# Kernel tuning notes

Hardware: AMD Instinct MI355X
Metric: run time of the kernel (lower is better)

Reference implementation:

```python
import jax, jax.numpy as jnp
import numpy as np
from jax import lax

B, C, T = 8, 512, 4096
K = 3
DILATIONS = (1, 3, 5)
EPS_Q = 1e-5
EPS_SNAKE = 1e-9


def quantize_weight(w):
    # BitNet-1.58-style ternary quantization with per-tensor absmean scale,
    # applied with a straight-through estimator.
    s = jnp.mean(jnp.abs(w))
    wq = jnp.clip(jnp.round(w / (s + EPS_Q)), -1.0, 1.0) * s
    return w + lax.stop_gradient(wq - w)


def bitconv1d(x, w, b, dilation, padding):
    # x: [B, C, T], w: [Cout, Cin, K], b: [Cout]
    y = lax.conv_general_dilated(
        x, quantize_weight(w),
        window_strides=(1,),
        padding=[(padding, padding)],
        rhs_dilation=(dilation,),
        dimension_numbers=("NCH", "OIH", "NCH"),
    )
    return y + b[None, :, None]


def snake_beta(x, alpha_p, beta_p):
    # log-scale parametrization: alpha = exp(alpha_p), beta = exp(beta_p)
    a = jnp.exp(alpha_p)[None, :, None]
    b = jnp.exp(beta_p)[None, :, None]
    return x + (1.0 / (b + EPS_SNAKE)) * jnp.sin(a * x) ** 2


def setup_inputs() -> dict:
    key = jax.random.key(0)
    ks = jax.random.split(key, 7)
    return {
        "x": jax.random.normal(ks[0], (B, C, T), dtype=jnp.float32),
        "w1": jax.random.normal(ks[1], (3, C, C, K), dtype=jnp.float32) * 0.05,
        "b1": jax.random.normal(ks[2], (3, C), dtype=jnp.float32) * 0.01,
        "alpha": jax.random.normal(ks[3], (3, C), dtype=jnp.float32) * 0.1,
        "beta": jax.random.normal(ks[4], (3, C), dtype=jnp.float32) * 0.1,
        "w2": jax.random.normal(ks[5], (3, C, C, K), dtype=jnp.float32) * 0.05,
        "b2": jax.random.normal(ks[6], (3, C), dtype=jnp.float32) * 0.01,
    }


def reference(x, w1, b1, alpha, beta, w2, b2):
    for i, d in enumerate(DILATIONS):
        pad1 = d * (K - 1) // 2
        h = bitconv1d(x, w1[i], b1[i], dilation=d, padding=pad1)
        h = snake_beta(h, alpha[i], beta[i])
        h = bitconv1d(h, w2[i], b2[i], dilation=1, padding=(K - 1) // 2)
        x = x + h
    return x
```

## Files before the change

kernel.cpp:

```cpp
#include <hip/hip_runtime.h>
#include <math.h>
#include <stdint.h>


constexpr int B_ = 8, C_ = 512, T_ = 4096, K_ = 3;
constexpr int WELEM = C_ * C_ * K_;

typedef __bf16 bf16x8 __attribute__((ext_vector_type(8)));
typedef float f32x4 __attribute__((ext_vector_type(4)));
typedef unsigned short u16x8 __attribute__((ext_vector_type(8)));

constexpr size_t OFF_PART = 0;
constexpr size_t OFF_S = 4096;
constexpr size_t OFF_AE = 8192;
constexpr size_t OFF_IB = 16384;
constexpr size_t OFF_WQ1 = 32768;
constexpr size_t OFF_WQ2 = OFF_WQ1 + (size_t)3 * WELEM * 2;
constexpr size_t NBCT = (size_t)B_ * C_ * T_;
constexpr size_t OFF_PHI = OFF_WQ2 + (size_t)3 * WELEM * 2;
constexpr size_t OFF_PLO = OFF_PHI + NBCT * 2;
constexpr size_t OFF_QHI = OFF_PLO + NBCT * 2;
constexpr size_t OFF_QLO = OFF_QHI + NBCT * 2;
constexpr size_t OFF_ZERO = OFF_QLO + NBCT * 2;

__device__ inline unsigned short bf16_rne(float v) {
  unsigned int u = __builtin_bit_cast(unsigned int, v);
  unsigned int r = u + 0x7FFFu + ((u >> 16) & 1u);
  return (unsigned short)(r >> 16);
}

__global__ __launch_bounds__(256)
void absmean_partial(const float* __restrict__ w1, const float* __restrict__ w2,
                     float* __restrict__ part) {
  __shared__ float red[256];
  const int t = blockIdx.y;
  const float* src = (t < 3) ? (w1 + (size_t)t * WELEM) : (w2 + (size_t)(t - 3) * WELEM);
  const int base = blockIdx.x * (256 * 32);
  float v = 0.f;
#pragma unroll
  for (int j = 0; j < 32; ++j) v += fabsf(src[base + j * 256 + threadIdx.x]);
  red[threadIdx.x] = v;
  __syncthreads();
  for (int s = 128; s > 0; s >>= 1) {
    if (threadIdx.x < (unsigned)s) red[threadIdx.x] += red[threadIdx.x + s];
    __syncthreads();
  }
  if (threadIdx.x == 0) part[t * 96 + blockIdx.x] = red[0];
}

__global__ __launch_bounds__(128)
void absmean_final(const float* __restrict__ part, float* __restrict__ svec) {
  __shared__ float red[128];
  const int t = blockIdx.x;
  red[threadIdx.x] = (threadIdx.x < 96) ? part[t * 96 + threadIdx.x] : 0.f;
  __syncthreads();
  for (int s = 64; s > 0; s >>= 1) {
    if (threadIdx.x < (unsigned)s) red[threadIdx.x] += red[threadIdx.x + s];
    __syncthreads();
  }
  if (threadIdx.x == 0) svec[t] = red[0] / (float)WELEM;
}

__global__ __launch_bounds__(256)
void quantize_kernel(const float* __restrict__ src, unsigned short* __restrict__ dst,
                     const float* __restrict__ svec, int sbase) {
  const int idx = blockIdx.x * 256 + threadIdx.x;
  const int j = idx & 7;
  const int lane = (idx >> 3) & 63;
  const int cot = (idx >> 9) & 31;
  const int rest = idx >> 14;
  const int tap = rest % 3;
  const int rest2 = rest / 3;
  const int cc = rest2 & 15;
  const int st = rest2 >> 4;
  const int co = cot * 16 + (lane & 15);
  const int ci = cc * 32 + (lane >> 4) * 8 + j;
  const float s = svec[sbase + st];
  const float w = src[(((size_t)st * C_ + co) * C_ + ci) * K_ + tap];
  float q = rintf(w / (s + 1e-5f));
  q = fminf(1.f, fmaxf(-1.f, q));
  dst[idx] = (unsigned short)(__builtin_bit_cast(unsigned int, q) >> 16);
}

__global__ __launch_bounds__(256)
void snake_params_kernel(const float* __restrict__ al, const float* __restrict__ be,
                         float* __restrict__ ae, float* __restrict__ ib,
                         float* __restrict__ zr) {
  const int idx = blockIdx.x * 256 + threadIdx.x;
  if (idx < 3 * C_) {
    ae[idx] = expf(al[idx]);
    ib[idx] = 1.f / (expf(be[idx]) + 1e-9f);
  }
  if (idx < 1024) zr[idx] = 0.f;
}

__global__ __launch_bounds__(256)
void transpose_split(const float* __restrict__ X, unsigned short* __restrict__ Hi,
                     unsigned short* __restrict__ Lo) {
  __shared__ float tile[64][68];
  const int b = blockIdx.z;
  const int c0 = blockIdx.y * 64;
  const int t0 = blockIdx.x * 64;
  const int tid = threadIdx.x;
  {
    const int cl = tid >> 2, tg = tid & 3;
    const float* src = X + ((size_t)b * C_ + c0 + cl) * T_ + t0 + tg * 16;
    float4 v0 = *(const float4*)(src);
    float4 v1 = *(const float4*)(src + 4);
    float4 v2 = *(const float4*)(src + 8);
    float4 v3 = *(const float4*)(src + 12);
    float* d = &tile[cl][tg * 16];
    *(float4*)(d) = v0; *(float4*)(d + 4) = v1;
    *(float4*)(d + 8) = v2; *(float4*)(d + 12) = v3;
  }
  __syncthreads();
  {
    const int tl = tid >> 2, cg = tid & 3;
    u16x8 h0, h1, l0, l1;
#pragma unroll
    for (int j = 0; j < 16; ++j) {
      const float v = tile[cg * 16 + j][tl];
      const unsigned short hb = bf16_rne(v);
      const float hf = __builtin_bit_cast(float, (unsigned int)hb << 16);
      const unsigned short lb = bf16_rne(v - hf);
      if (j < 8) { h0[j] = hb; l0[j] = lb; }
      else       { h1[j - 8] = hb; l1[j - 8] = lb; }
    }
    const size_t off = ((size_t)b * T_ + t0 + tl) * C_ + c0 + cg * 16;
    *(u16x8*)(Hi + off) = h0; *(u16x8*)(Hi + off + 8) = h1;
    *(u16x8*)(Lo + off) = l0; *(u16x8*)(Lo + off + 8) = l1;
  }
}

template <int DIL, bool SNAKE, bool PLANES, bool WF32>
__global__ __launch_bounds__(256, 2)
void conv_mfma(const unsigned short* __restrict__ Xhi,
               const unsigned short* __restrict__ Xlo,
               const unsigned short* __restrict__ Wq,
               unsigned int zoff,
               const float* __restrict__ svec,
               const float* __restrict__ bias, const float* __restrict__ aexp,
               const float* __restrict__ invb,
               const float* __restrict__ res,
               float* __restrict__ Y,
               unsigned short* __restrict__ Ohi,
               unsigned short* __restrict__ Olo) {
  constexpr int TT = 256;
  constexpr int R = TT + 2 * DIL;
  constexpr int R8 = (R + 7) & ~7;
  constexpr int W8 = R8 / 8;
  constexpr int NW = (W8 + 3) / 4;
  __shared__ unsigned short Xs[2][R8 * 64];

  const int b = blockIdx.z;
  const int co0 = blockIdx.y * 128;
  const int cob = blockIdx.y * 8;
  const int t0 = blockIdx.x * TT;
  const int tid = threadIdx.x;
  const int lane = tid & 63;
  const int wv = tid >> 6;
  const int l15 = lane & 15;
  const int quad = lane >> 4;

  f32x4 acc[8][4] = {};

  const size_t xbase = (size_t)b * T_ * C_;
  const unsigned int plo_delta = (unsigned int)(NBCT * 2);
  const char* xh8 = (const char*)Xhi;

  unsigned int offs[NW];
#pragma unroll
  for (int j = 0; j < NW; ++j) {
    const int wnd = wv + j * 4;
    const int rl = wnd * 8 + (lane >> 3);
    const int cpr = (lane & 7) ^ (rl & 7);
    const int p = cpr >> 2, g = cpr & 3;
    const int t = t0 - DIL + rl;
    unsigned int o;
    if (wnd < W8 && (unsigned)t < (unsigned)T_)
      o = (p ? plo_delta : 0u) + (unsigned int)((xbase + (size_t)t * C_ + g * 8) * 2);
    else
      o = zoff + (unsigned int)(g * 16);
    offs[j] = o;
  }

  auto stage = [&](int cc, int buf) {
#pragma unroll
    for (int j = 0; j < NW; ++j) {
      const int wnd = wv + j * 4;
      if (wnd < W8) {
        const char* gp = xh8 + offs[j] + cc * 64;
        __builtin_amdgcn_global_load_lds(
            (const __attribute__((address_space(1))) unsigned int*)gp,
            (__attribute__((address_space(3))) unsigned int*)&Xs[buf][wnd * 512],
            16, 0, 0);
      }
    }
  };

  stage(0, 0);
  __syncthreads();

#pragma unroll 1
  for (int cc = 0; cc < C_ / 32; ++cc) {
    const int cur = cc & 1;

    bf16x8 a0[8];
    {
      const unsigned short* wb =
          Wq + (((size_t)cc * K_ + 0) * 32 + cob) * 512 + (size_t)lane * 8;
#pragma unroll
      for (int m = 0; m < 8; ++m)
        a0[m] = __builtin_bit_cast(bf16x8, *(const u16x8*)(wb + m * 512));
    }

    if (cc < C_ / 32 - 1) stage(cc + 1, 1 - cur);

#pragma unroll
    for (int n = 0; n < 4; ++n) {
      const int r = wv * 64 + n * 16 + l15;
      const int rw = (r & 7) * 8;
      const bf16x8 bh =
          __builtin_bit_cast(bf16x8, *(const u16x8*)&Xs[cur][r * 64 + ((quad * 8) ^ rw)]);
      const bf16x8 bl =
          __builtin_bit_cast(bf16x8, *(const u16x8*)&Xs[cur][r * 64 + ((quad * 8 + 32) ^ rw)]);
#pragma unroll
      for (int m = 0; m < 8; ++m) {
        acc[m][n] = __builtin_amdgcn_mfma_f32_16x16x32_bf16(a0[m], bh, acc[m][n], 0, 0, 0);
        acc[m][n] = __builtin_amdgcn_mfma_f32_16x16x32_bf16(a0[m], bl, acc[m][n], 0, 0, 0);
      }
    }

#pragma unroll
    for (int tap = 1; tap < K_; ++tap) {
      const unsigned short* wb =
          Wq + (((size_t)cc * K_ + tap) * 32 + cob) * 512 + (size_t)lane * 8;
      bf16x8 a[8];
#pragma unroll
      for (int m = 0; m < 8; ++m)
        a[m] = __builtin_bit_cast(bf16x8, *(const u16x8*)(wb + m * 512));
#pragma unroll
      for (int n = 0; n < 4; ++n) {
        const int r = wv * 64 + n * 16 + l15 + tap * DIL;
        const int rw = (r & 7) * 8;
        const bf16x8 bh =
            __builtin_bit_cast(bf16x8, *(const u16x8*)&Xs[cur][r * 64 + ((quad * 8) ^ rw)]);
        const bf16x8 bl =
            __builtin_bit_cast(bf16x8, *(const u16x8*)&Xs[cur][r * 64 + ((quad * 8 + 32) ^ rw)]);
#pragma unroll
        for (int m = 0; m < 8; ++m) {
          acc[m][n] = __builtin_amdgcn_mfma_f32_16x16x32_bf16(a[m], bh, acc[m][n], 0, 0, 0);
          acc[m][n] = __builtin_amdgcn_mfma_f32_16x16x32_bf16(a[m], bl, acc[m][n], 0, 0, 0);
        }
      }
    }
    __syncthreads();
  }

  const float sw = *svec;

  if (PLANES) {
    uint32_t* E = (uint32_t*)&Xs[0][0];
    constexpr int ELD = 33;
#pragma unroll
    for (int mb = 0; mb < 4; ++mb) {
      __syncthreads();
#pragma unroll
      for (int mm = 0; mm < 2; ++mm) {
        const int m = mb * 2 + mm;
        const int cb = co0 + m * 16 + quad * 4;
        float bs[4], av[4], ibv[4];
#pragma unroll
        for (int reg = 0; reg < 4; ++reg) {
          bs[reg] = bias[cb + reg];
          if (SNAKE) { av[reg] = aexp[cb + reg]; ibv[reg] = invb[cb + reg]; }
        }
#pragma unroll
        for (int n = 0; n < 4; ++n) {
          const int tl = wv * 64 + n * 16 + l15;
          const int t = t0 + tl;
#pragma unroll
          for (int reg = 0; reg < 4; ++reg) {
            float v = sw * acc[m][n][reg] + bs[reg];
            if (SNAKE) {
              const float sn = __sinf(av[reg] * v);
              v = v + ibv[reg] * sn * sn;
            } else {
              v = v + res[((size_t)b * C_ + cb + reg) * T_ + t];
            }
            if (WF32) Y[((size_t)b * C_ + cb + reg) * T_ + t] = v;
            const unsigned short hb = bf16_rne(v);
            const float hf = __builtin_bit_cast(float, (unsigned int)hb << 16);
            const unsigned short lb = bf16_rne(v - hf);
            E[tl * ELD + mm * 16 + quad * 4 + reg] =
                ((unsigned int)hb << 16) | (unsigned int)lb;
          }
        }
      }
      __syncthreads();
      {
        const int row = tid;
        uint32_t u[32];
#pragma unroll
        for (int j = 0; j < 32; ++j) u[j] = E[row * ELD + j];
        u16x8 hq[4], lq[4];
#pragma unroll
        for (int g = 0; g < 4; ++g)
#pragma unroll
          for (int j = 0; j < 8; ++j) {
            hq[g][j] = (unsigned short)(u[g * 8 + j] >> 16);
            lq[g][j] = (unsigned short)(u[g * 8 + j] & 0xFFFFu);
          }
        const size_t poff = ((size_t)b * T_ + t0 + row) * C_ + co0 + mb * 32;
#pragma unroll
        for (int g = 0; g < 4; ++g) {
          *(u16x8*)(Ohi + poff + g * 8) = hq[g];
          *(u16x8*)(Olo + poff + g * 8) = lq[g];
        }
      }
    }
  } else {
#pragma unroll
    for (int m = 0; m < 8; ++m) {
      const int cb = co0 + m * 16 + quad * 4;
      float bs[4], av[4], ibv[4];
#pragma unroll
      for (int reg = 0; reg < 4; ++reg) {
        bs[reg] = bias[cb + reg];
        if (SNAKE) { av[reg] = aexp[cb + reg]; ibv[reg] = invb[cb + reg]; }
      }
#pragma unroll
      for (int n = 0; n < 4; ++n) {
        const int t = t0 + wv * 64 + n * 16 + l15;
#pragma unroll
        for (int reg = 0; reg < 4; ++reg) {
          float v = sw * acc[m][n][reg] + bs[reg];
          if (SNAKE) {
            const float sn = __sinf(av[reg] * v);
            v = v + ibv[reg] * sn * sn;
          } else {
            v = v + res[((size_t)b * C_ + cb + reg) * T_ + t];
          }
          Y[((size_t)b * C_ + cb + reg) * T_ + t] = v;
        }
      }
    }
  }
}

extern "C" void kernel_launch(void* const* d_in, const int* in_sizes, int n_in,
                              void* d_out, int out_size, void* d_ws, size_t ws_size,
                              hipStream_t stream) {
  (void)in_sizes; (void)n_in; (void)out_size; (void)ws_size;
  const float* x = (const float*)d_in[0];
  const float* w1 = (const float*)d_in[1];
  const float* b1 = (const float*)d_in[2];
  const float* al = (const float*)d_in[3];
  const float* be = (const float*)d_in[4];
  const float* w2 = (const float*)d_in[5];
  const float* b2 = (const float*)d_in[6];
  float* out = (float*)d_out;
  char* wsb = (char*)d_ws;

  float* part = (float*)(wsb + OFF_PART);
  float* svec = (float*)(wsb + OFF_S);
  float* ae = (float*)(wsb + OFF_AE);
  float* ib = (float*)(wsb + OFF_IB);
  unsigned short* wq1 = (unsigned short*)(wsb + OFF_WQ1);
  unsigned short* wq2 = (unsigned short*)(wsb + OFF_WQ2);
  unsigned short* Phi = (unsigned short*)(wsb + OFF_PHI);
  unsigned short* Plo = (unsigned short*)(wsb + OFF_PLO);
  unsigned short* Qhi = (unsigned short*)(wsb + OFF_QHI);
  unsigned short* Qlo = (unsigned short*)(wsb + OFF_QLO);
  float* zr = (float*)(wsb + OFF_ZERO);

  const unsigned int zoffP = (unsigned int)(OFF_ZERO - OFF_PHI);
  const unsigned int zoffQ = (unsigned int)(OFF_ZERO - OFF_QHI);

  absmean_partial<<<dim3(96, 6), 256, 0, stream>>>(w1, w2, part);
  absmean_final<<<6, 128, 0, stream>>>(part, svec);
  quantize_kernel<<<(3 * WELEM) / 256, 256, 0, stream>>>(w1, wq1, svec, 0);
  quantize_kernel<<<(3 * WELEM) / 256, 256, 0, stream>>>(w2, wq2, svec, 3);
  snake_params_kernel<<<6, 256, 0, stream>>>(al, be, ae, ib, zr);

  const dim3 tgrid(T_ / 64, C_ / 64, B_);
  const dim3 cgrid(T_ / 256, C_ / 128, B_);

  transpose_split<<<tgrid, 256, 0, stream>>>(x, Phi, Plo);

  conv_mfma<1, true, true, false><<<cgrid, 256, 0, stream>>>(
      Phi, Plo, wq1 + 0 * (size_t)WELEM, zoffP, svec + 0, b1 + 0, ae + 0, ib + 0,
      nullptr, nullptr, Qhi, Qlo);
  conv_mfma<1, false, true, true><<<cgrid, 256, 0, stream>>>(
      Qhi, Qlo, wq2 + 0 * (size_t)WELEM, zoffQ, svec + 3, b2 + 0, nullptr, nullptr,
      x, out, Phi, Plo);

  conv_mfma<3, true, true, false><<<cgrid, 256, 0, stream>>>(
      Phi, Plo, wq1 + 1 * (size_t)WELEM, zoffP, svec + 1, b1 + C_, ae + C_, ib + C_,
      nullptr, nullptr, Qhi, Qlo);
  conv_mfma<1, false, true, true><<<cgrid, 256, 0, stream>>>(
      Qhi, Qlo, wq2 + 1 * (size_t)WELEM, zoffQ, svec + 4, b2 + C_, nullptr, nullptr,
      out, out, Phi, Plo);

  conv_mfma<5, true, true, false><<<cgrid, 256, 0, stream>>>(
      Phi, Plo, wq1 + 2 * (size_t)WELEM, zoffP, svec + 2, b1 + 2 * C_, ae + 2 * C_,
      ib + 2 * C_, nullptr, nullptr, Qhi, Qlo);
  conv_mfma<1, false, false, true><<<cgrid, 256, 0, stream>>>(
      Qhi, Qlo, wq2 + 2 * (size_t)WELEM, zoffQ, svec + 5, b2 + 2 * C_, nullptr, nullptr,
      out, out, nullptr, nullptr);
}
```

Before: 748.9 us.

## Halve time tile and split waves 2x2 over channels and time

Shrinks the conv time tile from 256 to 128 and arranges the four waves as a 2x2 grid over output channels and time, so each wave holds a 64x64 accumulator tile instead of 128x64. Launch bounds are raised to allow four blocks per CU and the grid doubles along time. The goal is lower register pressure, more blocks in flight and more concurrent work to hide latency. The cost is a larger share of halo rows per tile, more weight loads per output, and an epilogue reworked to stage through LDS in two passes.

```diff
diff --git a/kernel.cpp b/kernel.cpp
--- a/kernel.cpp
+++ b/kernel.cpp
@@ -133,7 +133,7 @@
 }
 
 template <int DIL, bool SNAKE, bool PLANES, bool WF32>
-__global__ __launch_bounds__(256, 2)
+__global__ __launch_bounds__(256, 4)
 void conv_mfma(const unsigned short* __restrict__ Xhi,
                const unsigned short* __restrict__ Xlo,
                const unsigned short* __restrict__ Wq,
@@ -145,7 +145,7 @@
                float* __restrict__ Y,
                unsigned short* __restrict__ Ohi,
                unsigned short* __restrict__ Olo) {
-  constexpr int TT = 256;
+  constexpr int TT = 128;
   constexpr int R = TT + 2 * DIL;
   constexpr int R8 = (R + 7) & ~7;
   constexpr int W8 = R8 / 8;
@@ -159,10 +159,12 @@
   const int tid = threadIdx.x;
   const int lane = tid & 63;
   const int wv = tid >> 6;
+  const int wm = wv >> 1;
+  const int wt = wv & 1;
   const int l15 = lane & 15;
   const int quad = lane >> 4;
 
-  f32x4 acc[8][4] = {};
+  f32x4 acc[4][4] = {};
 
   const size_t xbase = (size_t)b * T_ * C_;
   const unsigned int plo_delta = (unsigned int)(NBCT * 2);
@@ -205,12 +207,12 @@
   for (int cc = 0; cc < C_ / 32; ++cc) {
     const int cur = cc & 1;
 
-    bf16x8 a0[8];
+    bf16x8 a0[4];
     {
       const unsigned short* wb =
-          Wq + (((size_t)cc * K_ + 0) * 32 + cob) * 512 + (size_t)lane * 8;
-#pragma unroll
-      for (int m = 0; m < 8; ++m)
+          Wq + (((size_t)cc * K_ + 0) * 32 + cob + wm * 4) * 512 + (size_t)lane * 8;
+#pragma unroll
+      for (int m = 0; m < 4; ++m)
         a0[m] = __builtin_bit_cast(bf16x8, *(const u16x8*)(wb + m * 512));
     }
 
@@ -218,14 +220,14 @@
 
 #pragma unroll
     for (int n = 0; n < 4; ++n) {
-      const int r = wv * 64 + n * 16 + l15;
+      const int r = wt * 64 + n * 16 + l15;
       const int rw = (r & 7) * 8;
       const bf16x8 bh =
           __builtin_bit_cast(bf16x8, *(const u16x8*)&Xs[cur][r * 64 + ((quad * 8) ^ rw)]);
       const bf16x8 bl =
           __builtin_bit_cast(bf16x8, *(const u16x8*)&Xs[cur][r * 64 + ((quad * 8 + 32) ^ rw)]);
 #pragma unroll
-      for (int m = 0; m < 8; ++m) {
+      for (int m = 0; m < 4; ++m) {
         acc[m][n] = __builtin_amdgcn_mfma_f32_16x16x32_bf16(a0[m], bh, acc[m][n], 0, 0, 0);
         acc[m][n] = __builtin_amdgcn_mfma_f32_16x16x32_bf16(a0[m], bl, acc[m][n], 0, 0, 0);
       }
@@ -234,21 +236,21 @@
 #pragma unroll
     for (int tap = 1; tap < K_; ++tap) {
       const unsigned short* wb =
-          Wq + (((size_t)cc * K_ + tap) * 32 + cob) * 512 + (size_t)lane * 8;
-      bf16x8 a[8];
-#pragma unroll
-      for (int m = 0; m < 8; ++m)
+          Wq + (((size_t)cc * K_ + tap) * 32 + cob + wm * 4) * 512 + (size_t)lane * 8;
+      bf16x8 a[4];
+#pragma unroll
+      for (int m = 0; m < 4; ++m)
         a[m] = __builtin_bit_cast(bf16x8, *(const u16x8*)(wb + m * 512));
 #pragma unroll
       for (int n = 0; n < 4; ++n) {
-        const int r = wv * 64 + n * 16 + l15 + tap * DIL;
+        const int r = wt * 64 + n * 16 + l15 + tap * DIL;
         const int rw = (r & 7) * 8;
         const bf16x8 bh =
             __builtin_bit_cast(bf16x8, *(const u16x8*)&Xs[cur][r * 64 + ((quad * 8) ^ rw)]);
         const bf16x8 bl =
             __builtin_bit_cast(bf16x8, *(const u16x8*)&Xs[cur][r * 64 + ((quad * 8 + 32) ^ rw)]);
 #pragma unroll
-        for (int m = 0; m < 8; ++m) {
+        for (int m = 0; m < 4; ++m) {
           acc[m][n] = __builtin_amdgcn_mfma_f32_16x16x32_bf16(a[m], bh, acc[m][n], 0, 0, 0);
           acc[m][n] = __builtin_amdgcn_mfma_f32_16x16x32_bf16(a[m], bl, acc[m][n], 0, 0, 0);
         }
@@ -261,68 +263,74 @@
 
   if (PLANES) {
     uint32_t* E = (uint32_t*)&Xs[0][0];
-    constexpr int ELD = 33;
-#pragma unroll
-    for (int mb = 0; mb < 4; ++mb) {
+    constexpr int ELD = 65;
+#pragma unroll
+    for (int mb = 0; mb < 2; ++mb) {
       __syncthreads();
-#pragma unroll
-      for (int mm = 0; mm < 2; ++mm) {
-        const int m = mb * 2 + mm;
-        const int cb = co0 + m * 16 + quad * 4;
-        float bs[4], av[4], ibv[4];
-#pragma unroll
-        for (int reg = 0; reg < 4; ++reg) {
-          bs[reg] = bias[cb + reg];
-          if (SNAKE) { av[reg] = aexp[cb + reg]; ibv[reg] = invb[cb + reg]; }
-        }
-#pragma unroll
-        for (int n = 0; n < 4; ++n) {
-          const int tl = wv * 64 + n * 16 + l15;
-          const int t = t0 + tl;
+      if (wm == mb) {
+#pragma unroll
+        for (int m = 0; m < 4; ++m) {
+          const int cb = co0 + mb * 64 + m * 16 + quad * 4;
+          float bs[4], av[4], ibv[4];
 #pragma unroll
           for (int reg = 0; reg < 4; ++reg) {
-            float v = sw * acc[m][n][reg] + bs[reg];
-            if (SNAKE) {
-              const float sn = __sinf(av[reg] * v);
-              v = v + ibv[reg] * sn * sn;
-            } else {
-              v = v + res[((size_t)b * C_ + cb + reg) * T_ + t];
+            bs[reg] = bias[cb + reg];
+            if (SNAKE) { av[reg] = aexp[cb + reg]; ibv[reg] = invb[cb + reg]; }
+          }
+#pragma unroll
+          for (int n = 0; n < 4; ++n) {
+            const int tl = wt * 64 + n * 16 + l15;
+            const int t = t0 + tl;
+#pragma unroll
+            for (int reg = 0; reg < 4; ++reg) {
+              float v = sw * acc[m][n][reg] + bs[reg];
+              if (SNAKE) {
+                const float sn = __sinf(av[reg] * v);
+                v = v + ibv[reg] * sn * sn;
+              } else {
+                v = v + res[((size_t)b * C_ + cb + reg) * T_ + t];
+              }
+              if (WF32) Y[((size_t)b * C_ + cb + reg) * T_ + t] = v;
+              const unsigned short hb = bf16_rne(v);
+              const float hf = __builtin_bit_cast(float, (unsigned int)hb << 16);
+              const unsigned short lb = bf16_rne(v - hf);
+              E[tl * ELD + m * 16 + quad * 4 + reg] =
+                  ((unsigned int)hb << 16) | (unsigned int)lb;
             }
-            if (WF32) Y[((size_t)b * C_ + cb + reg) * T_ + t] = v;
-            const unsigned short hb = bf16_rne(v);
-            const float hf = __builtin_bit_cast(float, (unsigned int)hb << 16);
-            const unsigned short lb = bf16_rne(v - hf);
-            E[tl * ELD + mm * 16 + quad * 4 + reg] =
-                ((unsigned int)hb << 16) | (unsigned int)lb;
           }
         }
       }
       __syncthreads();
       {
-        const int row = tid;
-        uint32_t u[32];
-#pragma unroll
-        for (int j = 0; j < 32; ++j) u[j] = E[row * ELD + j];
-        u16x8 hq[4], lq[4];
-#pragma unroll
-        for (int g = 0; g < 4; ++g)
-#pragma unroll
-          for (int j = 0; j < 8; ++j) {
-            hq[g][j] = (unsigned short)(u[g * 8 + j] >> 16);
-            lq[g][j] = (unsigned short)(u[g * 8 + j] & 0xFFFFu);
+        const int row = tid >> 1;
+        const int half = tid & 1;
+        const size_t poff =
+            ((size_t)b * T_ + t0 + row) * C_ + co0 + mb * 64 + half * 32;
+#pragma unroll
+        for (int h2 = 0; h2 < 2; ++h2) {
+          uint32_t u[16];
+#pragma unroll
+          for (int j = 0; j < 16; ++j) u[j] = E[row * ELD + half * 32 + h2 * 16 + j];
+          u16x8 hq[2], lq[2];
+#pragma unroll
+          for (int g = 0; g < 2; ++g)
+#pragma unroll
+            for (int j = 0; j < 8; ++j) {
+              hq[g][j] = (unsigned short)(u[g * 8 + j] >> 16);
+              lq[g][j] = (unsigned short)(u[g * 8 + j] & 0xFFFFu);
+            }
+#pragma unroll
+          for (int g = 0; g < 2; ++g) {
+            *(u16x8*)(Ohi + poff + h2 * 16 + g * 8) = hq[g];
+            *(u16x8*)(Olo + poff + h2 * 16 + g * 8) = lq[g];
           }
-        const size_t poff = ((size_t)b * T_ + t0 + row) * C_ + co0 + mb * 32;
-#pragma unroll
-        for (int g = 0; g < 4; ++g) {
-          *(u16x8*)(Ohi + poff + g * 8) = hq[g];
-          *(u16x8*)(Olo + poff + g * 8) = lq[g];
         }
       }
     }
   } else {
 #pragma unroll
-    for (int m = 0; m < 8; ++m) {
-      const int cb = co0 + m * 16 + quad * 4;
+    for (int m = 0; m < 4; ++m) {
+      const int cb = co0 + wm * 64 + m * 16 + quad * 4;
       float bs[4], av[4], ibv[4];
 #pragma unroll
       for (int reg = 0; reg < 4; ++reg) {
@@ -331,7 +339,7 @@
       }
 #pragma unroll
       for (int n = 0; n < 4; ++n) {
-        const int t = t0 + wv * 64 + n * 16 + l15;
+        const int t = t0 + wt * 64 + n * 16 + l15;
 #pragma unroll
         for (int reg = 0; reg < 4; ++reg) {
           float v = sw * acc[m][n][reg] + bs[reg];
@@ -384,7 +392,7 @@
   snake_params_kernel<<<6, 256, 0, stream>>>(al, be, ae, ib, zr);
 
   const dim3 tgrid(T_ / 64, C_ / 64, B_);
-  const dim3 cgrid(T_ / 256, C_ / 128, B_);
+  const dim3 cgrid(T_ / 128, C_ / 128, B_);
 
   transpose_split<<<tgrid, 256, 0, stream>>>(x, Phi, Plo);
 
```

Result: slower. 893.0 us (+19.2%).

## Give each wave a private LDS halo tile and drop block-wide barriers

Applied to the files above, without the earlier changes.

Restructures the conv K-loop so each of the four waves stages its own 64-row time slice plus dilation halo into a private LDS region. Each wave then waits on its own async global-to-LDS loads with explicit vmcnt counts, so the per-iteration __syncthreads goes away. The up-front tap-0 weight preload is also folded back into the uniform tap loop. The cost is duplicated halo loads and slightly more LDS per block, and correctness now depends on hand-tuned vmcnt values matching the number of issued loads.

```diff
diff --git a/kernel.cpp b/kernel.cpp
--- a/kernel.cpp
+++ b/kernel.cpp
@@ -146,11 +146,11 @@
                unsigned short* __restrict__ Ohi,
                unsigned short* __restrict__ Olo) {
   constexpr int TT = 256;
-  constexpr int R = TT + 2 * DIL;
-  constexpr int R8 = (R + 7) & ~7;
-  constexpr int W8 = R8 / 8;
-  constexpr int NW = (W8 + 3) / 4;
-  __shared__ unsigned short Xs[2][R8 * 64];
+  constexpr int RW = 64 + 2 * DIL;
+  constexpr int FW = RW / 8;
+  constexpr int REM = RW % 8;
+  constexpr int NWW = FW + (REM ? 1 : 0);
+  __shared__ unsigned short Xs[2][4][RW * 64];
 
   const int b = blockIdx.z;
   const int co0 = blockIdx.y * 128;
@@ -168,16 +168,15 @@
   const unsigned int plo_delta = (unsigned int)(NBCT * 2);
   const char* xh8 = (const char*)Xhi;
 
-  unsigned int offs[NW];
-#pragma unroll
-  for (int j = 0; j < NW; ++j) {
-    const int wnd = wv + j * 4;
-    const int rl = wnd * 8 + (lane >> 3);
+  unsigned int offs[NWW];
+#pragma unroll
+  for (int j = 0; j < NWW; ++j) {
+    const int rl = j * 8 + (lane >> 3);
     const int cpr = (lane & 7) ^ (rl & 7);
     const int p = cpr >> 2, g = cpr & 3;
-    const int t = t0 - DIL + rl;
+    const int t = t0 + wv * 64 - DIL + rl;
     unsigned int o;
-    if (wnd < W8 && (unsigned)t < (unsigned)T_)
+    if (rl < RW && (unsigned)t < (unsigned)T_)
       o = (p ? plo_delta : 0u) + (unsigned int)((xbase + (size_t)t * C_ + g * 8) * 2);
     else
       o = zoff + (unsigned int)(g * 16);
@@ -186,53 +185,38 @@
 
   auto stage = [&](int cc, int buf) {
 #pragma unroll
-    for (int j = 0; j < NW; ++j) {
-      const int wnd = wv + j * 4;
-      if (wnd < W8) {
-        const char* gp = xh8 + offs[j] + cc * 64;
+    for (int j = 0; j < NWW; ++j) {
+      const char* gp = xh8 + offs[j] + cc * 64;
+      auto dst = (__attribute__((address_space(3))) unsigned int*)&Xs[buf][wv][j * 512];
+      if (j < FW) {
         __builtin_amdgcn_global_load_lds(
-            (const __attribute__((address_space(1))) unsigned int*)gp,
-            (__attribute__((address_space(3))) unsigned int*)&Xs[buf][wnd * 512],
-            16, 0, 0);
+            (const __attribute__((address_space(1))) unsigned int*)gp, dst, 16, 0, 0);
+      } else if ((lane >> 3) < REM) {
+        __builtin_amdgcn_global_load_lds(
+            (const __attribute__((address_space(1))) unsigned int*)gp, dst, 16, 0, 0);
       }
     }
   };
 
   stage(0, 0);
-  __syncthreads();
 
 #pragma unroll 1
   for (int cc = 0; cc < C_ / 32; ++cc) {
     const int cur = cc & 1;
 
-    bf16x8 a0[8];
-    {
-      const unsigned short* wb =
-          Wq + (((size_t)cc * K_ + 0) * 32 + cob) * 512 + (size_t)lane * 8;
-#pragma unroll
-      for (int m = 0; m < 8; ++m)
-        a0[m] = __builtin_bit_cast(bf16x8, *(const u16x8*)(wb + m * 512));
-    }
-
-    if (cc < C_ / 32 - 1) stage(cc + 1, 1 - cur);
-
-#pragma unroll
-    for (int n = 0; n < 4; ++n) {
-      const int r = wv * 64 + n * 16 + l15;
-      const int rw = (r & 7) * 8;
-      const bf16x8 bh =
-          __builtin_bit_cast(bf16x8, *(const u16x8*)&Xs[cur][r * 64 + ((quad * 8) ^ rw)]);
-      const bf16x8 bl =
-          __builtin_bit_cast(bf16x8, *(const u16x8*)&Xs[cur][r * 64 + ((quad * 8 + 32) ^ rw)]);
-#pragma unroll
-      for (int m = 0; m < 8; ++m) {
-        acc[m][n] = __builtin_amdgcn_mfma_f32_16x16x32_bf16(a0[m], bh, acc[m][n], 0, 0, 0);
-        acc[m][n] = __builtin_amdgcn_mfma_f32_16x16x32_bf16(a0[m], bl, acc[m][n], 0, 0, 0);
-      }
-    }
-
-#pragma unroll
-    for (int tap = 1; tap < K_; ++tap) {
+    __builtin_amdgcn_sched_barrier(0);
+    if (cc < C_ / 32 - 1) {
+      stage(cc + 1, 1 - cur);
+      if constexpr (NWW == 9)       asm volatile("s_waitcnt vmcnt(9)" ::: "memory");
+      else if constexpr (NWW == 10) asm volatile("s_waitcnt vmcnt(10)" ::: "memory");
+      else                          asm volatile("s_waitcnt vmcnt(0)" ::: "memory");
+    } else {
+      asm volatile("s_waitcnt vmcnt(0)" ::: "memory");
+    }
+    __builtin_amdgcn_sched_barrier(0);
+
+#pragma unroll
+    for (int tap = 0; tap < K_; ++tap) {
       const unsigned short* wb =
           Wq + (((size_t)cc * K_ + tap) * 32 + cob) * 512 + (size_t)lane * 8;
       bf16x8 a[8];
@@ -241,12 +225,12 @@
         a[m] = __builtin_bit_cast(bf16x8, *(const u16x8*)(wb + m * 512));
 #pragma unroll
       for (int n = 0; n < 4; ++n) {
-        const int r = wv * 64 + n * 16 + l15 + tap * DIL;
+        const int r = n * 16 + l15 + tap * DIL;
         const int rw = (r & 7) * 8;
-        const bf16x8 bh =
-            __builtin_bit_cast(bf16x8, *(const u16x8*)&Xs[cur][r * 64 + ((quad * 8) ^ rw)]);
-        const bf16x8 bl =
-            __builtin_bit_cast(bf16x8, *(const u16x8*)&Xs[cur][r * 64 + ((quad * 8 + 32) ^ rw)]);
+        const bf16x8 bh = __builtin_bit_cast(
+            bf16x8, *(const u16x8*)&Xs[cur][wv][r * 64 + ((quad * 8) ^ rw)]);
+        const bf16x8 bl = __builtin_bit_cast(
+            bf16x8, *(const u16x8*)&Xs[cur][wv][r * 64 + ((quad * 8 + 32) ^ rw)]);
 #pragma unroll
         for (int m = 0; m < 8; ++m) {
           acc[m][n] = __builtin_amdgcn_mfma_f32_16x16x32_bf16(a[m], bh, acc[m][n], 0, 0, 0);
@@ -254,13 +238,12 @@
         }
       }
     }
-    __syncthreads();
   }
 
   const float sw = *svec;
 
   if (PLANES) {
-    uint32_t* E = (uint32_t*)&Xs[0][0];
+    uint32_t* E = (uint32_t*)&Xs[0][0][0];
     constexpr int ELD = 33;
 #pragma unroll
     for (int mb = 0; mb < 4; ++mb) {
```

Measured after the change: 814.8 us. +8.8%, slower.
